# Optimization experiments

Measured on AMD Instinct MI355X. Metric: run time of the kernel, lower is better.

Reference implementation:

```python
import jax, jax.numpy as jnp
import numpy as np

D_MODEL = 512
N_HEADS = 8
HEAD_DIM = D_MODEL // N_HEADS
NEG_INF = -1e9


def setup_inputs() -> dict:
    key = jax.random.key(0)
    ks = jax.random.split(key, 12)
    B, N, M = 8, 2048, 2048
    inp = {
        'query': jax.random.normal(ks[0], (B, D_MODEL, N), jnp.float32),
        'key': jax.random.normal(ks[1], (B, D_MODEL, M), jnp.float32),
        'value': jax.random.normal(ks[2], (B, D_MODEL, M), jnp.float32),
        'query_mask': jnp.ones((B, N), jnp.float32),
        'key_value_mask': jnp.ones((B, M), jnp.float32),
        # Conv1d(d_model, d_model, kernel_size=1) == pointwise linear: W [out, in], b [out]
        'Wq': jax.random.normal(ks[3], (D_MODEL, D_MODEL), jnp.float32) / np.sqrt(D_MODEL),
        'bq': jax.random.normal(ks[4], (D_MODEL,), jnp.float32) * 0.01,
        'Wk': jax.random.normal(ks[5], (D_MODEL, D_MODEL), jnp.float32) / np.sqrt(D_MODEL),
        'bk': jax.random.normal(ks[6], (D_MODEL,), jnp.float32) * 0.01,
        'Wv': jax.random.normal(ks[7], (D_MODEL, D_MODEL), jnp.float32) / np.sqrt(D_MODEL),
        'bv': jax.random.normal(ks[8], (D_MODEL,), jnp.float32) * 0.01,
        'Wm': jax.random.normal(ks[9], (D_MODEL, D_MODEL), jnp.float32) / np.sqrt(D_MODEL),
        'bm': jax.random.normal(ks[10], (D_MODEL,), jnp.float32) * 0.01,
    }
    return inp


def _pointwise(W, b, x):
    # Conv1d k=1 over [B, C_in, N] -> [B, C_out, N]
    return jnp.einsum('oi,bin->bon', W, x) + b[None, :, None]


def reference(query, key, value, query_mask, key_value_mask,
              Wq, bq, Wk, bk, Wv, bv, Wm, bm):
    B = query.shape[0]
    N = query.shape[2]
    M = key.shape[2]
    # project and split heads: [B, head_dim, n_heads, seq]
    q = _pointwise(Wq, bq, query).reshape(B, HEAD_DIM, N_HEADS, N)
    k = _pointwise(Wk, bk, key).reshape(B, HEAD_DIM, N_HEADS, M)
    v = _pointwise(Wv, bv, value).reshape(B, HEAD_DIM, N_HEADS, M)
    # scores [B, H, N, M], scaled by sqrt(head_dim) (query.shape[1] post-split)
    scores = jnp.einsum('bdhn,bdhm->bhnm', q, k) / jnp.sqrt(jnp.float32(HEAD_DIM))
    # dual mask: outer product of key_value_mask [B,1,1,M] and query_mask [B,1,N,1]
    mask = key_value_mask[:, None, None, :] * query_mask[:, None, :, None]
    scores = jnp.where(mask > 0, scores, NEG_INF)
    prob = jax.nn.softmax(scores, axis=-1)  # [B, H, N, M]
    x = jnp.einsum('bhnm,bdhm->bdhn', prob, v)  # [B, head_dim, H, N]
    out = _pointwise(Wm, bm, x.reshape(B, D_MODEL, N))
    return out
```

## Files before the change

kernel.cpp:

```cpp
#include <hip/hip_runtime.h>


typedef _Float16 f16;
typedef _Float16 f16x4 __attribute__((ext_vector_type(4)));
typedef _Float16 f16x8 __attribute__((ext_vector_type(8)));
typedef float f32x4 __attribute__((ext_vector_type(4)));

#define D_MODEL 512
#define HD 64
#define SEQ 2048
#define QSCL 0.18033688011112042f
#define KVNEG -1.4426950409e9f

__global__ __launch_bounds__(256) void k_transpose(
    const float* __restrict__ q, const float* __restrict__ k, const float* __restrict__ v,
    f16* __restrict__ XT)
{
  __shared__ __align__(16) f16 Ts[64][72];
  int t = threadIdx.x;
  int nt = blockIdx.x, ct = blockIdx.y, z = blockIdx.z;
  int src = z >> 3, b = z & 7;
  const float* S = (src == 0) ? q : (src == 1) ? k : v;
  {
    int cr = t >> 2, ns = t & 3;
    const float* p = S + ((size_t)b * D_MODEL + ct * 64 + cr) * SEQ + nt * 64 + ns * 16;
    f32x4 a0 = *(const f32x4*)(p);
    f32x4 a1 = *(const f32x4*)(p + 4);
    f32x4 a2 = *(const f32x4*)(p + 8);
    f32x4 a3 = *(const f32x4*)(p + 12);
    f16x8 h0, h1;
#pragma unroll
    for (int j = 0; j < 4; ++j) { h0[j] = (f16)a0[j]; h0[4 + j] = (f16)a1[j]; h1[j] = (f16)a2[j]; h1[4 + j] = (f16)a3[j]; }
    *(f16x8*)&Ts[cr][ns * 16] = h0;
    *(f16x8*)&Ts[cr][ns * 16 + 8] = h1;
  }
  __syncthreads();
  {
    int nr = t >> 2, cs = t & 3;
    f16x8 h0, h1;
#pragma unroll
    for (int j = 0; j < 8; ++j) h0[j] = Ts[cs * 16 + j][nr];
#pragma unroll
    for (int j = 0; j < 8; ++j) h1[j] = Ts[cs * 16 + 8 + j][nr];
    f16* dst = XT + (((size_t)z) * SEQ + nt * 64 + nr) * D_MODEL + ct * 64 + cs * 16;
    *(f16x8*)dst = h0;
    *(f16x8*)(dst + 8) = h1;
  }
}

__global__ __launch_bounds__(256) void k_wconv(
    const float* __restrict__ Wq, const float* __restrict__ Wk, const float* __restrict__ Wv,
    const float* __restrict__ Wm, f16* __restrict__ W3, f16* __restrict__ Wmh)
{
  int idx = blockIdx.x * 256 + threadIdx.x;
  if (idx < 262144) {
    W3[idx] = (f16)Wq[idx];
    W3[262144 + idx] = (f16)Wk[idx];
    W3[524288 + idx] = (f16)Wv[idx];
    int o = idx >> 9, c = idx & 511;
    int h = c & 7, d = c >> 3;
    Wmh[((size_t)h * 512 + o) * 64 + d] = (f16)Wm[idx];
  }
}

__global__ __launch_bounds__(256, 2) void k_proj(
    const f16* __restrict__ W3, const float* __restrict__ bq, const float* __restrict__ bk,
    const float* __restrict__ bv, const f16* __restrict__ XT,
    f16* __restrict__ Qt, f16* __restrict__ Kt, f16* __restrict__ Vh)
{
  __shared__ __align__(16) char smem[34816];
  f16 (*As)[40] = (f16(*)[40])smem;
  f16 (*Bs)[40] = (f16(*)[40])(smem + 10240);
  f16 (*Ls)[136] = (f16(*)[136])smem;

  int t = threadIdx.x;
  int proj = blockIdx.z, b = blockIdx.y;
  int ot = blockIdx.x & 3, ntile = blockIdx.x >> 2;
  int w = t >> 6, ln = t & 63, i16 = ln & 15, q4 = ln >> 4;
  int ow = w >> 1, nw = w & 1;

  const f16* Wp = W3 + (size_t)proj * 262144;
  const f16* Xp = XT + ((size_t)proj * 8 + b) * (size_t)SEQ * D_MODEL;

  f32x4 acc[4][4];
#pragma unroll
  for (int x = 0; x < 4; ++x)
#pragma unroll
    for (int y = 0; y < 4; ++y) acc[x][y] = (f32x4){0.f, 0.f, 0.f, 0.f};

  int srow = t >> 1, sseg = t & 1;
  for (int kc = 0; kc < 16; ++kc) {
    __syncthreads();
    const f16* Ap = Wp + ((size_t)(ot * 128 + srow)) * 512 + kc * 32 + sseg * 16;
    *(f32x4*)&As[srow][sseg * 16] = *(const f32x4*)(Ap);
    *(f32x4*)&As[srow][sseg * 16 + 8] = *(const f32x4*)(Ap + 8);
    const f16* Bp = Xp + ((size_t)(ntile * 128 + srow)) * 512 + kc * 32 + sseg * 16;
    *(f32x4*)&Bs[srow][sseg * 16] = *(const f32x4*)(Bp);
    *(f32x4*)&Bs[srow][sseg * 16 + 8] = *(const f32x4*)(Bp + 8);
    __syncthreads();
    f16x8 af[4], bf[4];
#pragma unroll
    for (int x = 0; x < 4; ++x) af[x] = *(const f16x8*)&As[ow * 64 + x * 16 + i16][q4 * 8];
#pragma unroll
    for (int y = 0; y < 4; ++y) bf[y] = *(const f16x8*)&Bs[nw * 64 + y * 16 + i16][q4 * 8];
#pragma unroll
    for (int x = 0; x < 4; ++x)
#pragma unroll
      for (int y = 0; y < 4; ++y)
        acc[x][y] = __builtin_amdgcn_mfma_f32_16x16x32_f16(af[x], bf[y], acc[x][y], 0, 0, 0);
  }

  const float* bias = (proj == 0) ? bq : (proj == 1) ? bk : bv;
  float scl = (proj == 0) ? QSCL : 1.0f;
  __syncthreads();
#pragma unroll
  for (int x = 0; x < 4; ++x) {
    f32x4 bb = *(const f32x4*)(bias + ot * 128 + ow * 64 + x * 16 + q4 * 4);
#pragma unroll
    for (int y = 0; y < 4; ++y)
#pragma unroll
      for (int r = 0; r < 4; ++r)
        Ls[ow * 64 + x * 16 + q4 * 4 + r][nw * 64 + y * 16 + i16] = (f16)((acc[x][y][r] + bb[r]) * scl);
  }
  __syncthreads();
  if (proj < 2) {
    f16* dst = (proj == 0) ? Qt : Kt;
#pragma unroll
    for (int rnd = 0; rnd < 4; ++rnd) {
      int task = rnd * 256 + t;
      int nl = task & 127, h = task >> 7;
      f16x8 g0, g1;
#pragma unroll
      for (int j = 0; j < 8; ++j) g0[j] = Ls[8 * j + h][nl];
#pragma unroll
      for (int j = 0; j < 8; ++j) g1[j] = Ls[8 * (8 + j) + h][nl];
      f16* dp = dst + (((size_t)(b * 8 + h)) * SEQ + ntile * 128 + nl) * HD + ot * 16;
      *(f16x8*)dp = g0;
      *(f16x8*)(dp + 8) = g1;
    }
  } else {
#pragma unroll
    for (int p = 0; p < 8; ++p) {
      int ol = (t >> 4) + 16 * p;
      int ch = t & 15;
      int og = ot * 128 + ol;
      int h = og & 7, d = og >> 3;
      f16* dp = Vh + (((size_t)(b * 8 + h)) * HD + d) * SEQ + ntile * 128 + ch * 8;
      *(f32x4*)dp = *(const f32x4*)&Ls[ol][ch * 8];
    }
  }
}

__global__ __launch_bounds__(256, 4) void k_attn(
    const f16* __restrict__ Qt, const f16* __restrict__ Kt, const f16* __restrict__ Vh,
    const float* __restrict__ qmask, const float* __restrict__ kvmask,
    f16* __restrict__ O)
{
  __shared__ __align__(16) char smem[18688];
  f16 (*Qs)[72] = (f16(*)[72])smem;
  f16 (*Ks)[72] = (f16(*)[72])smem;
  f16 (*Vs)[72] = (f16(*)[72])(smem + 9216);
  float* kvb = (float*)(smem + 18432);

  int t = threadIdx.x;
  int bh = blockIdx.x >> 4;
  int b = bh >> 3;
  int n0 = (blockIdx.x & 15) * 128;
  int w = t >> 6, ln = t & 63, i16 = ln & 15, q4 = ln >> 4;

  const f16* Qb = Qt + (size_t)bh * SEQ * HD;
  const f16* Kb = Kt + (size_t)bh * SEQ * HD;
  const f16* Vb = Vh + (size_t)bh * HD * SEQ;

#pragma unroll
  for (int p = 0; p < 4; ++p) {
    int row = (t >> 3) + 32 * p, ch = t & 7;
    *(f32x4*)&Qs[row][ch * 8] = *(const f32x4*)(Qb + ((size_t)(n0 + row)) * HD + ch * 8);
  }
  __syncthreads();
  f16x8 qf[2][2];
#pragma unroll
  for (int nt = 0; nt < 2; ++nt)
#pragma unroll
    for (int kc = 0; kc < 2; ++kc)
      qf[nt][kc] = *(const f16x8*)&Qs[w * 32 + nt * 16 + i16][kc * 32 + q4 * 8];
  float qok[2];
#pragma unroll
  for (int nt = 0; nt < 2; ++nt)
    qok[nt] = qmask[(size_t)b * SEQ + n0 + w * 32 + nt * 16 + i16];

  f32x4 acc_o[4][2];
#pragma unroll
  for (int dt = 0; dt < 4; ++dt)
#pragma unroll
    for (int nt = 0; nt < 2; ++nt) acc_o[dt][nt] = (f32x4){0.f, 0.f, 0.f, 0.f};
  float m_i[2] = {-3e38f, -3e38f};
  float l_i[2] = {0.f, 0.f};

  for (int it = 0; it < 32; ++it) {
    int m0 = it * 64;
    __syncthreads();
#pragma unroll
    for (int p = 0; p < 2; ++p) {
      int row = (t >> 3) + 32 * p, ch = t & 7;
      *(f32x4*)&Ks[row][ch * 8] = *(const f32x4*)(Kb + ((size_t)(m0 + row)) * HD + ch * 8);
      *(f32x4*)&Vs[row][ch * 8] = *(const f32x4*)(Vb + ((size_t)row) * SEQ + m0 + ch * 8);
    }
    if (t < 64) {
      float kv = kvmask[(size_t)b * SEQ + m0 + t];
      kvb[t] = (kv > 0.f) ? 0.f : KVNEG;
    }
    __syncthreads();

    f16x8 kf[4][2];
#pragma unroll
    for (int mt = 0; mt < 4; ++mt)
#pragma unroll
      for (int kc = 0; kc < 2; ++kc)
        kf[mt][kc] = *(const f16x8*)&Ks[mt * 16 + i16][kc * 32 + q4 * 8];
    f32x4 kvf[4];
#pragma unroll
    for (int mt = 0; mt < 4; ++mt) kvf[mt] = *(const f32x4*)&kvb[mt * 16 + q4 * 4];

    f16x4 pf[4][2];
    float al[2];
#pragma unroll
    for (int nt = 0; nt < 2; ++nt) {
      f32x4 s[4];
#pragma unroll
      for (int mt = 0; mt < 4; ++mt) {
        f32x4 a = kvf[mt];
        a = __builtin_amdgcn_mfma_f32_16x16x32_f16(kf[mt][0], qf[nt][0], a, 0, 0, 0);
        a = __builtin_amdgcn_mfma_f32_16x16x32_f16(kf[mt][1], qf[nt][1], a, 0, 0, 0);
        s[mt] = a;
      }
      bool qz = qok[nt] > 0.f;
      float mx = -3e38f;
#pragma unroll
      for (int mt = 0; mt < 4; ++mt)
#pragma unroll
        for (int r = 0; r < 4; ++r) {
          float sv = qz ? s[mt][r] : KVNEG;
          s[mt][r] = sv;
          mx = fmaxf(mx, sv);
        }
      mx = fmaxf(mx, __shfl_xor(mx, 16, 64));
      mx = fmaxf(mx, __shfl_xor(mx, 32, 64));
      float mnew = fmaxf(m_i[nt], mx);
      float alpha = __builtin_amdgcn_exp2f(m_i[nt] - mnew);
      float rsum = 0.f;
#pragma unroll
      for (int mt = 0; mt < 4; ++mt) {
        float p0 = __builtin_amdgcn_exp2f(s[mt][0] - mnew);
        float p1 = __builtin_amdgcn_exp2f(s[mt][1] - mnew);
        float p2 = __builtin_amdgcn_exp2f(s[mt][2] - mnew);
        float p3 = __builtin_amdgcn_exp2f(s[mt][3] - mnew);
        rsum += (p0 + p1) + (p2 + p3);
        f16x4 pv;
        pv[0] = (f16)p0; pv[1] = (f16)p1; pv[2] = (f16)p2; pv[3] = (f16)p3;
        pf[mt][nt] = pv;
      }
      rsum += __shfl_xor(rsum, 16, 64);
      rsum += __shfl_xor(rsum, 32, 64);
      l_i[nt] = l_i[nt] * alpha + rsum;
      m_i[nt] = mnew;
      al[nt] = alpha;
    }

    f16x4 vf[4][4];
#pragma unroll
    for (int dt = 0; dt < 4; ++dt)
#pragma unroll
      for (int mt = 0; mt < 4; ++mt)
        vf[dt][mt] = *(const f16x4*)&Vs[dt * 16 + i16][mt * 16 + q4 * 4];

#pragma unroll
    for (int dt = 0; dt < 4; ++dt)
#pragma unroll
      for (int nt = 0; nt < 2; ++nt) {
        f32x4 o = acc_o[dt][nt];
        float a = al[nt];
#pragma unroll
        for (int r = 0; r < 4; ++r) o[r] *= a;
#pragma unroll
        for (int mt = 0; mt < 4; ++mt)
          o = __builtin_amdgcn_mfma_f32_16x16x16f16(vf[dt][mt], pf[mt][nt], o, 0, 0, 0);
        acc_o[dt][nt] = o;
      }
  }

  __syncthreads();
  f16 (*Os)[72] = (f16(*)[72])(smem + w * 4608);
#pragma unroll
  for (int nt = 0; nt < 2; ++nt) {
    float inv = 1.f / l_i[nt];
#pragma unroll
    for (int dt = 0; dt < 4; ++dt) {
      f16x4 o4;
#pragma unroll
      for (int r = 0; r < 4; ++r) o4[r] = (f16)(acc_o[dt][nt][r] * inv);
      *(f16x4*)&Os[nt * 16 + i16][dt * 16 + q4 * 4] = o4;
    }
  }
  __syncthreads();
  f16* Ob = O + ((size_t)bh * SEQ + n0 + w * 32) * HD;
#pragma unroll
  for (int p = 0; p < 4; ++p) {
    int row = (ln >> 3) + 8 * p, ch = ln & 7;
    *(f32x4*)(Ob + (size_t)row * HD + ch * 8) = *(const f32x4*)&Os[row][ch * 8];
  }
}

__global__ __launch_bounds__(256, 2) void k_out(
    const f16* __restrict__ Wmh, const float* __restrict__ bm,
    const f16* __restrict__ O, float* __restrict__ out)
{
  __shared__ __align__(16) char smem[20480];
  f16 (*As)[40] = (f16(*)[40])smem;
  f16 (*Bs)[40] = (f16(*)[40])(smem + 10240);

  int t = threadIdx.x;
  int b = blockIdx.y;
  int ot = blockIdx.x & 3, ntile = blockIdx.x >> 2;
  int w = t >> 6, ln = t & 63, i16 = ln & 15, q4 = ln >> 4;
  int ow = w >> 1, nw = w & 1;

  f32x4 acc[4][4];
#pragma unroll
  for (int x = 0; x < 4; ++x)
#pragma unroll
    for (int y = 0; y < 4; ++y) acc[x][y] = (f32x4){0.f, 0.f, 0.f, 0.f};

  int srow = t >> 1, sseg = t & 1;
  for (int ck = 0; ck < 16; ++ck) {
    int h = ck >> 1, dc = ck & 1;
    __syncthreads();
    const f16* Ap = Wmh + ((size_t)h * 512 + ot * 128 + srow) * 64 + dc * 32 + sseg * 16;
    *(f32x4*)&As[srow][sseg * 16] = *(const f32x4*)(Ap);
    *(f32x4*)&As[srow][sseg * 16 + 8] = *(const f32x4*)(Ap + 8);
    const f16* Bp = O + (((size_t)(b * 8 + h)) * SEQ + ntile * 128 + srow) * 64 + dc * 32 + sseg * 16;
    *(f32x4*)&Bs[srow][sseg * 16] = *(const f32x4*)(Bp);
    *(f32x4*)&Bs[srow][sseg * 16 + 8] = *(const f32x4*)(Bp + 8);
    __syncthreads();
    f16x8 af[4], bf[4];
#pragma unroll
    for (int x = 0; x < 4; ++x) af[x] = *(const f16x8*)&As[ow * 64 + x * 16 + i16][q4 * 8];
#pragma unroll
    for (int y = 0; y < 4; ++y) bf[y] = *(const f16x8*)&Bs[nw * 64 + y * 16 + i16][q4 * 8];
#pragma unroll
    for (int x = 0; x < 4; ++x)
#pragma unroll
      for (int y = 0; y < 4; ++y)
        acc[x][y] = __builtin_amdgcn_mfma_f32_16x16x32_f16(af[x], bf[y], acc[x][y], 0, 0, 0);
  }

#pragma unroll
  for (int x = 0; x < 4; ++x) {
    f32x4 bb = *(const f32x4*)(bm + ot * 128 + ow * 64 + x * 16 + q4 * 4);
#pragma unroll
    for (int y = 0; y < 4; ++y)
#pragma unroll
      for (int r = 0; r < 4; ++r) {
        int o_g = ot * 128 + ow * 64 + x * 16 + q4 * 4 + r;
        int n_g = ntile * 128 + nw * 64 + y * 16 + i16;
        out[((size_t)b * 512 + o_g) * SEQ + n_g] = acc[x][y][r] + bb[r];
      }
  }
}

extern "C" void kernel_launch(void* const* d_in, const int* in_sizes, int n_in,
                              void* d_out, int out_size, void* d_ws, size_t ws_size,
                              hipStream_t stream)
{
  const float* query  = (const float*)d_in[0];
  const float* key    = (const float*)d_in[1];
  const float* value  = (const float*)d_in[2];
  const float* qmask  = (const float*)d_in[3];
  const float* kvmask = (const float*)d_in[4];
  const float* Wq = (const float*)d_in[5];
  const float* bq = (const float*)d_in[6];
  const float* Wk = (const float*)d_in[7];
  const float* bk = (const float*)d_in[8];
  const float* Wv = (const float*)d_in[9];
  const float* bv = (const float*)d_in[10];
  const float* Wm = (const float*)d_in[11];
  const float* bm = (const float*)d_in[12];
  float* out = (float*)d_out;

  char* ws = (char*)d_ws;
  f16* XT  = (f16*)(ws);
  f16* Qt  = (f16*)(ws + 50331648);
  f16* Kt  = (f16*)(ws + 67108864);
  f16* Vh  = (f16*)(ws + 83886080);
  f16* Oat = (f16*)(ws);
  f16* W3  = (f16*)(ws + 100663296);
  f16* Wmh = (f16*)(ws + 102236160);

  k_transpose<<<dim3(32, 8, 24), 256, 0, stream>>>(query, key, value, XT);
  k_wconv<<<1024, 256, 0, stream>>>(Wq, Wk, Wv, Wm, W3, Wmh);
  k_proj<<<dim3(64, 8, 3), 256, 0, stream>>>(W3, bq, bk, bv, XT, Qt, Kt, Vh);
  k_attn<<<1024, 256, 0, stream>>>(Qt, Kt, Vh, qmask, kvmask, Oat);
  k_out<<<dim3(64, 8), 256, 0, stream>>>(Wmh, bm, Oat, out);
}
```

Baseline: 356.1 us.

## Prefetch K/V tiles into registers and retile Q/K layout into 16-wide chunks

The attention loop now loads the next K/V tile into registers while the current tile is being computed, then stores it to shared memory after a barrier. This is meant to hide global-load latency behind the MFMA work. The Q/K projection output is rearranged into a [bh][chunk4][seq][16] layout so that projection stores and attention loads are more contiguous. The query mask is folded into the Q fragments by zeroing them, which removes the per-element select in the softmax. The register prefetch raises register pressure, and zeroing masked Q rows gives uniform scores instead of -1e9, which changes the result for masked queries.

```diff
diff --git a/kernel.cpp b/kernel.cpp
--- a/kernel.cpp
+++ b/kernel.cpp
@@ -125,18 +125,14 @@
   __syncthreads();
   if (proj < 2) {
     f16* dst = (proj == 0) ? Qt : Kt;
-#pragma unroll
-    for (int rnd = 0; rnd < 4; ++rnd) {
-      int task = rnd * 256 + t;
-      int nl = task & 127, h = task >> 7;
-      f16x8 g0, g1;
-#pragma unroll
-      for (int j = 0; j < 8; ++j) g0[j] = Ls[8 * j + h][nl];
-#pragma unroll
-      for (int j = 0; j < 8; ++j) g1[j] = Ls[8 * (8 + j) + h][nl];
-      f16* dp = dst + (((size_t)(b * 8 + h)) * SEQ + ntile * 128 + nl) * HD + ot * 16;
-      *(f16x8*)dp = g0;
-      *(f16x8*)(dp + 8) = g1;
+    int n = t >> 1, seg = t & 1;
+#pragma unroll
+    for (int h = 0; h < 8; ++h) {
+      f16x8 g;
+#pragma unroll
+      for (int j = 0; j < 8; ++j) g[j] = Ls[8 * (seg * 8 + j) + h][n];
+      f16* dp = dst + (((size_t)((b * 8 + h) * 4 + ot)) * 2048 + ntile * 128 + n) * 16 + seg * 8;
+      *(f16x8*)dp = g;
     }
   } else {
 #pragma unroll
@@ -168,14 +164,16 @@
   int n0 = (blockIdx.x & 15) * 128;
   int w = t >> 6, ln = t & 63, i16 = ln & 15, q4 = ln >> 4;
 
-  const f16* Qb = Qt + (size_t)bh * SEQ * HD;
-  const f16* Kb = Kt + (size_t)bh * SEQ * HD;
+  const f16* Qb = Qt + (size_t)bh * 131072;
+  const f16* Kb = Kt + (size_t)bh * 131072;
   const f16* Vb = Vh + (size_t)bh * HD * SEQ;
 
 #pragma unroll
   for (int p = 0; p < 4; ++p) {
-    int row = (t >> 3) + 32 * p, ch = t & 7;
-    *(f32x4*)&Qs[row][ch * 8] = *(const f32x4*)(Qb + ((size_t)(n0 + row)) * HD + ch * 8);
+    int tid = p * 256 + t;
+    int n = tid & 127, cx = tid >> 7;
+    *(f32x4*)&Qs[n][cx * 8] =
+        *(const f32x4*)(Qb + ((size_t)((cx >> 1) * 2048 + n0 + n)) * 16 + (cx & 1) * 8);
   }
   __syncthreads();
   f16x8 qf[2][2];
@@ -184,10 +182,13 @@
 #pragma unroll
     for (int kc = 0; kc < 2; ++kc)
       qf[nt][kc] = *(const f16x8*)&Qs[w * 32 + nt * 16 + i16][kc * 32 + q4 * 8];
-  float qok[2];
-#pragma unroll
-  for (int nt = 0; nt < 2; ++nt)
-    qok[nt] = qmask[(size_t)b * SEQ + n0 + w * 32 + nt * 16 + i16];
+#pragma unroll
+  for (int nt = 0; nt < 2; ++nt) {
+    float qok = qmask[(size_t)b * SEQ + n0 + w * 32 + nt * 16 + i16];
+    f16 qz = (qok > 0.f) ? (f16)1 : (f16)0;
+    qf[nt][0] *= qz;
+    qf[nt][1] *= qz;
+  }
 
   f32x4 acc_o[4][2];
 #pragma unroll
@@ -197,21 +198,32 @@
   float m_i[2] = {-3e38f, -3e38f};
   float l_i[2] = {0.f, 0.f};
 
-  for (int it = 0; it < 32; ++it) {
+  f32x4 kr0[2], vr0[2], kr1[2], vr1[2];
+  float kv0, kv1;
+
+  auto issue = [&](int it, f32x4* kr, f32x4* vr, float& kv) {
     int m0 = it * 64;
-    __syncthreads();
 #pragma unroll
     for (int p = 0; p < 2; ++p) {
-      int row = (t >> 3) + 32 * p, ch = t & 7;
-      *(f32x4*)&Ks[row][ch * 8] = *(const f32x4*)(Kb + ((size_t)(m0 + row)) * HD + ch * 8);
-      *(f32x4*)&Vs[row][ch * 8] = *(const f32x4*)(Vb + ((size_t)row) * SEQ + m0 + ch * 8);
-    }
-    if (t < 64) {
-      float kv = kvmask[(size_t)b * SEQ + m0 + t];
-      kvb[t] = (kv > 0.f) ? 0.f : KVNEG;
-    }
-    __syncthreads();
-
+      int tid = p * 256 + t;
+      int cx = tid >> 6, nk = tid & 63;
+      kr[p] = *(const f32x4*)(Kb + ((size_t)((cx >> 1) * 2048 + m0 + nk)) * 16 + (cx & 1) * 8);
+      vr[p] = *(const f32x4*)(Vb + ((size_t)(tid >> 3)) * SEQ + m0 + (tid & 7) * 8);
+    }
+    kv = kvmask[(size_t)b * SEQ + m0 + (t & 63)];
+  };
+
+  auto store = [&](const f32x4* kr, const f32x4* vr, float kv) {
+#pragma unroll
+    for (int p = 0; p < 2; ++p) {
+      int tid = p * 256 + t;
+      *(f32x4*)&Ks[tid & 63][(tid >> 6) * 8] = kr[p];
+      *(f32x4*)&Vs[tid >> 3][(tid & 7) * 8] = vr[p];
+    }
+    if (t < 64) kvb[t] = (kv > 0.f) ? 0.f : KVNEG;
+  };
+
+  auto compute = [&]() {
     f16x8 kf[4][2];
 #pragma unroll
     for (int mt = 0; mt < 4; ++mt)
@@ -234,16 +246,10 @@
         a = __builtin_amdgcn_mfma_f32_16x16x32_f16(kf[mt][1], qf[nt][1], a, 0, 0, 0);
         s[mt] = a;
       }
-      bool qz = qok[nt] > 0.f;
-      float mx = -3e38f;
-#pragma unroll
-      for (int mt = 0; mt < 4; ++mt)
-#pragma unroll
-        for (int r = 0; r < 4; ++r) {
-          float sv = qz ? s[mt][r] : KVNEG;
-          s[mt][r] = sv;
-          mx = fmaxf(mx, sv);
-        }
+      float mx = fmaxf(fmaxf(s[0][0], s[0][1]), fmaxf(s[0][2], s[0][3]));
+#pragma unroll
+      for (int mt = 1; mt < 4; ++mt)
+        mx = fmaxf(mx, fmaxf(fmaxf(s[mt][0], s[mt][1]), fmaxf(s[mt][2], s[mt][3])));
       mx = fmaxf(mx, __shfl_xor(mx, 16, 64));
       mx = fmaxf(mx, __shfl_xor(mx, 32, 64));
       float mnew = fmaxf(m_i[nt], mx);
@@ -267,15 +273,12 @@
       al[nt] = alpha;
     }
 
-    f16x4 vf[4][4];
-#pragma unroll
-    for (int dt = 0; dt < 4; ++dt)
+#pragma unroll
+    for (int dt = 0; dt < 4; ++dt) {
+      f16x4 vf[4];
 #pragma unroll
       for (int mt = 0; mt < 4; ++mt)
-        vf[dt][mt] = *(const f16x4*)&Vs[dt * 16 + i16][mt * 16 + q4 * 4];
-
-#pragma unroll
-    for (int dt = 0; dt < 4; ++dt)
+        vf[mt] = *(const f16x4*)&Vs[dt * 16 + i16][mt * 16 + q4 * 4];
 #pragma unroll
       for (int nt = 0; nt < 2; ++nt) {
         f32x4 o = acc_o[dt][nt];
@@ -284,9 +287,24 @@
         for (int r = 0; r < 4; ++r) o[r] *= a;
 #pragma unroll
         for (int mt = 0; mt < 4; ++mt)
-          o = __builtin_amdgcn_mfma_f32_16x16x16f16(vf[dt][mt], pf[mt][nt], o, 0, 0, 0);
+          o = __builtin_amdgcn_mfma_f32_16x16x16f16(vf[mt], pf[mt][nt], o, 0, 0, 0);
         acc_o[dt][nt] = o;
       }
+    }
+  };
+
+  issue(0, kr0, vr0, kv0);
+  for (int it = 0; it < 32; it += 2) {
+    __syncthreads();
+    store(kr0, vr0, kv0);
+    issue(it + 1, kr1, vr1, kv1);
+    __syncthreads();
+    compute();
+    __syncthreads();
+    store(kr1, vr1, kv1);
+    if (it + 2 < 32) issue(it + 2, kr0, vr0, kv0);
+    __syncthreads();
+    compute();
   }
 
   __syncthreads();
```

Measured after the change: 580.3 us. +63.0%, slower.
